# Performance work log

Hardware: AMD Instinct MI355X
Metric: run time of the kernel (lower is better)

Reference implementation:

```python
import jax, jax.numpy as jnp
import numpy as np

B, L, D, H = 2, 2048, 1024, 16
DH = D // H


def setup_inputs() -> dict:
    key = jax.random.key(0)
    ks = jax.random.split(key, 5)
    bound = 1.0 / D ** 0.5
    x = jax.random.normal(ks[0], (B, L, D), dtype=jnp.float32)
    # causal mask: 0 means masked out
    mask = jnp.tril(jnp.ones((L, L), dtype=jnp.int32))[None].repeat(B, axis=0)
    Wq = jax.random.uniform(ks[1], (D, D), jnp.float32, -bound, bound)
    Wk = jax.random.uniform(ks[2], (D, D), jnp.float32, -bound, bound)
    Wv = jax.random.uniform(ks[3], (D, D), jnp.float32, -bound, bound)
    Wo = jax.random.uniform(ks[4], (D, D), jnp.float32, -bound, bound)
    return {"x": x, "mask": mask, "Wq": Wq, "Wk": Wk, "Wv": Wv, "Wo": Wo}


def _split_heads(t):
    # (B, L, D) -> (B, H, L, DH)
    b, l, _ = t.shape
    return t.reshape(b, l, H, DH).transpose(0, 2, 1, 3)


def reference(x, mask, Wq, Wk, Wv, Wo):
    # projections: torch Linear does x @ W.T with W:(out,in)
    q = _split_heads(x @ Wq.T)  # (B,H,L,DH)
    k = _split_heads(x @ Wk.T)
    v = _split_heads(x @ Wv.T)
    scores = jnp.einsum('bhqd,bhkd->bhqk', q, k) / jnp.sqrt(jnp.float32(DH))
    m = mask[:, None, :, :]  # (B,1,L,L)
    scores = jnp.where(m == 0, jnp.float32(-jnp.inf), scores)
    attn = jax.nn.softmax(scores, axis=-1)
    out = jnp.einsum('bhqk,bhkd->bhqd', attn, v)  # (B,H,L,DH)
    out = out.transpose(0, 2, 1, 3).reshape(x.shape[0], x.shape[1], D)
    return out @ Wo.T
```

## Files before the change

kernel.cpp:

```cpp
#include <hip/hip_runtime.h>
#include <stdint.h>


typedef unsigned short u16;
typedef __attribute__((ext_vector_type(8))) short short8;
typedef __attribute__((ext_vector_type(4))) float f32x4;
typedef __attribute__((ext_vector_type(4))) unsigned int uint4v;

#define NEG_BIG (-1e30f)
#define QSCALE 0.18033688011112042f

__device__ __forceinline__ f32x4 mfma16(short8 a, short8 b, f32x4 c) {
    return __builtin_amdgcn_mfma_f32_16x16x32_bf16(a, b, c, 0, 0, 0);
}

__device__ __forceinline__ u16 f2bf(float f) {
    uint32_t u = __float_as_uint(f);
    u += 0x7fffu + ((u >> 16) & 1u);
    return (u16)(u >> 16);
}

#if __has_builtin(__builtin_amdgcn_cvt_pk_bf16_f32)
__device__ __forceinline__ unsigned int f2bf_pk(float a, float b) {
    return __builtin_bit_cast(unsigned int, __builtin_amdgcn_cvt_pk_bf16_f32(a, b));
}
#else
__device__ __forceinline__ unsigned int f2bf_pk(float a, float b) {
    return (unsigned int)f2bf(a) | ((unsigned int)f2bf(b) << 16);
}
#endif

__device__ __forceinline__ void load_lds_16B(const u16* g, u16* lds_base) {
    __builtin_amdgcn_global_load_lds(
        (__attribute__((address_space(1))) void*)(uintptr_t)(const void*)g,
        (__attribute__((address_space(3))) void*)lds_base,
        16, 0, 0);
}

__global__ __launch_bounds__(256) void cvt_kernel(
    const float* __restrict__ x, const float* __restrict__ wq, const float* __restrict__ wk,
    const float* __restrict__ wv, const float* __restrict__ wo, u16* __restrict__ dst)
{
    const int gid = blockIdx.x * 256 + threadIdx.x;
    const float* src; size_t off;
    if (gid < 524288)      { src = x;  off = (size_t)gid * 8; }
    else if (gid < 655360) { src = wq; off = (size_t)(gid - 524288) * 8; }
    else if (gid < 786432) { src = wk; off = (size_t)(gid - 655360) * 8; }
    else if (gid < 917504) { src = wv; off = (size_t)(gid - 786432) * 8; }
    else                   { src = wo; off = (size_t)(gid - 917504) * 8; }
    float4 a = *(const float4*)(src + off);
    float4 b = *(const float4*)(src + off + 4);
    uint4v u = { f2bf_pk(a.x, a.y), f2bf_pk(a.z, a.w),
                 f2bf_pk(b.x, b.y), f2bf_pk(b.z, b.w) };
    *(uint4v*)(dst + (size_t)gid * 8) = u;
}

__device__ __forceinline__ void gemm_bt_128x128_bk64(
    const u16* __restrict__ A, const u16* __restrict__ Bw,
    u16* at, u16* bt, int m0, int n0, f32x4 acc[4][4])
{
    const int tid  = threadIdx.x;
    const int w    = tid >> 6, lane = tid & 63;
    const int quad = lane >> 4, l15 = lane & 15;
    const int wm   = (w >> 1) * 64, wn = (w & 1) * 64;
    const int srow = lane >> 3;
    const int sch  = lane & 7;

    for (int k0 = 0; k0 < 1024; k0 += 64) {
#pragma unroll
        for (int c = 0; c < 4; ++c) {
            int row = w * 32 + c * 8 + srow;
            int g   = sch ^ (row & 7);
            load_lds_16B(A  + (size_t)(m0 + row) * 1024 + k0 + g * 8, at + (w * 32 + c * 8) * 64);
            load_lds_16B(Bw + (size_t)(n0 + row) * 1024 + k0 + g * 8, bt + (w * 32 + c * 8) * 64);
        }
        __syncthreads();
#pragma unroll
        for (int ks = 0; ks < 2; ++ks) {
            short8 af[4], bf[4];
#pragma unroll
            for (int rf = 0; rf < 4; ++rf) {
                int ra = wm + rf * 16 + l15, pa = (ks * 4 + quad) ^ (ra & 7);
                af[rf] = *(const short8*)(at + ra * 64 + pa * 8);
                int rb = wn + rf * 16 + l15, pb = (ks * 4 + quad) ^ (rb & 7);
                bf[rf] = *(const short8*)(bt + rb * 64 + pb * 8);
            }
#pragma unroll
            for (int rf = 0; rf < 4; ++rf)
#pragma unroll
                for (int cf = 0; cf < 4; ++cf)
                    acc[rf][cf] = mfma16(af[rf], bf[cf], acc[rf][cf]);
        }
        __syncthreads();
    }
}

__global__ __launch_bounds__(256, 3) void qkv_gemm(
    const u16* __restrict__ xb, const u16* __restrict__ Wq, const u16* __restrict__ Wk,
    const u16* __restrict__ Wv, u16* __restrict__ qbuf, u16* __restrict__ kbuf,
    u16* __restrict__ vtbuf)
{
    __shared__ __align__(16) u16 at[128 * 64];
    __shared__ __align__(16) u16 bt[128 * 64];
    const int m0  = blockIdx.x * 128;
    const int by  = blockIdx.y;
    const int sel = by >> 3;
    const int n0  = (by & 7) * 128;
    const u16* Wsel = sel == 0 ? Wq : (sel == 1 ? Wk : Wv);

    f32x4 acc[4][4];
    const f32x4 z = {0.f, 0.f, 0.f, 0.f};
#pragma unroll
    for (int i = 0; i < 4; ++i)
#pragma unroll
        for (int j = 0; j < 4; ++j) acc[i][j] = z;

    gemm_bt_128x128_bk64(xb, Wsel, at, bt, m0, n0, acc);

    const int tid  = threadIdx.x, w = tid >> 6, lane = tid & 63;
    const int quad = lane >> 4, l15 = lane & 15;
    const int wm   = (w >> 1) * 64, wn = (w & 1) * 64;

    if (sel < 2) {
        u16* dst = sel == 0 ? qbuf : kbuf;
        const float scl = sel == 0 ? QSCALE : 1.0f;
#pragma unroll
        for (int rf = 0; rf < 4; ++rf)
#pragma unroll
            for (int cf = 0; cf < 4; ++cf) {
                int n = n0 + wn + cf * 16 + l15;
                int h = n >> 6, dh = n & 63;
#pragma unroll
                for (int r = 0; r < 4; ++r) {
                    int m = m0 + wm + rf * 16 + quad * 4 + r;
                    int b = m >> 11, l = m & 2047;
                    dst[(((size_t)(b * 16 + h)) * 2048 + l) * 64 + dh] = f2bf(acc[rf][cf][r] * scl);
                }
            }
    } else {
#pragma unroll
        for (int rf = 0; rf < 4; ++rf)
#pragma unroll
            for (int cf = 0; cf < 4; ++cf) {
                int n = n0 + wn + cf * 16 + l15;
                int h = n >> 6, dh = n & 63;
                int m = m0 + wm + rf * 16 + quad * 4;
                int b = m >> 11, l = m & 2047;
                ushort4 pk;
                pk.x = f2bf(acc[rf][cf][0]);
                pk.y = f2bf(acc[rf][cf][1]);
                pk.z = f2bf(acc[rf][cf][2]);
                pk.w = f2bf(acc[rf][cf][3]);
                *(ushort4*)(vtbuf + (((size_t)(b * 16 + h)) * 64 + dh) * 2048 + l) = pk;
            }
    }
}

__global__ __launch_bounds__(256, 4) void attn_kernel(
    const u16* __restrict__ qbuf, const u16* __restrict__ kbuf,
    const u16* __restrict__ vtbuf, u16* __restrict__ attn)
{
    __shared__ __align__(16) u16 kt[2][64 * 64];
    __shared__ __align__(16) u16 vt[2][64 * 64];
    __shared__ __align__(16) u16 pt[4 * 16 * 64];

    const int tid  = threadIdx.x, w = tid >> 6, lane = tid & 63;
    const int quad = lane >> 4, l15 = lane & 15;
    const int bh   = blockIdx.y;
    const int jq   = ((blockIdx.y >> 3) & 1) ? (int)blockIdx.x : (31 - (int)blockIdx.x);
    const int q0   = jq * 64;
    const int qw   = q0 + w * 16;

    const u16* qbase = qbuf  + (size_t)bh * 2048 * 64;
    const u16* kbase = kbuf  + (size_t)bh * 2048 * 64;
    const u16* vbase = vtbuf + (size_t)bh * 64 * 2048;
    u16* pw = pt + w * (16 * 64);
    const int b = bh >> 4, h = bh & 15;

    const f32x4 z = {0.f, 0.f, 0.f, 0.f};

    short8 qf[2];
#pragma unroll
    for (int ks = 0; ks < 2; ++ks)
        qf[ks] = *(const short8*)(qbase + (size_t)(qw + l15) * 64 + ks * 32 + quad * 8);

    f32x4 o[4];
    float mrun = NEG_BIG, lrun = 0.f;
#pragma unroll
    for (int df = 0; df < 4; ++df) o[df] = z;

    auto stage = [&](int t, int buf) {
        const int k0 = t * 64;
#pragma unroll
        for (int c = 0; c < 2; ++c) {
            int row = w * 16 + c * 8 + (lane >> 3);
            int g   = (lane & 7) ^ (row & 7);
            load_lds_16B(kbase + (size_t)(k0 + row) * 64 + g * 8, kt[buf] + (w * 16 + c * 8) * 64);
            load_lds_16B(vbase + (size_t)row * 2048 + k0 + g * 8, vt[buf] + (w * 16 + c * 8) * 64);
        }
    };

    const int ntiles = jq + 1;
    stage(0, 0);
    for (int t = 0; t < ntiles; ++t) {
        __syncthreads();
        if (t + 1 < ntiles) stage(t + 1, (t + 1) & 1);
        const int k0 = t * 64;
        if (k0 <= qw + 15) {
            const u16* ktb = kt[t & 1];
            const u16* vtb = vt[t & 1];
            f32x4 st[4];
#pragma unroll
            for (int nf = 0; nf < 4; ++nf) st[nf] = z;
#pragma unroll
            for (int ks = 0; ks < 2; ++ks)
#pragma unroll
                for (int nf = 0; nf < 4; ++nf) {
                    int row = nf * 16 + l15;
                    int ph  = (ks * 4 + quad) ^ (row & 7);
                    short8 kf = *(const short8*)(ktb + row * 64 + ph * 8);
                    st[nf] = mfma16(kf, qf[ks], st[nf]);
                }
            if (k0 + 63 > qw) {
                int qrow = qw + l15;
#pragma unroll
                for (int nf = 0; nf < 4; ++nf)
#pragma unroll
                    for (int r = 0; r < 4; ++r) {
                        int key = k0 + nf * 16 + quad * 4 + r;
                        if (key > qrow) st[nf][r] = NEG_BIG;
                    }
            }
            {
                float mx = st[0][0];
#pragma unroll
                for (int nf = 0; nf < 4; ++nf)
#pragma unroll
                    for (int r = 0; r < 4; ++r) mx = fmaxf(mx, st[nf][r]);
                mx = fmaxf(mx, __shfl_xor(mx, 16));
                mx = fmaxf(mx, __shfl_xor(mx, 32));
                float mnew = fmaxf(mrun, mx);
                float alpha = exp2f(mrun - mnew);
                float sum = 0.f;
#pragma unroll
                for (int nf = 0; nf < 4; ++nf)
#pragma unroll
                    for (int r = 0; r < 4; ++r) {
                        float p = exp2f(st[nf][r] - mnew);
                        st[nf][r] = p;
                        sum += p;
                    }
                sum += __shfl_xor(sum, 16);
                sum += __shfl_xor(sum, 32);
                lrun = lrun * alpha + sum;
                mrun = mnew;
#pragma unroll
                for (int df = 0; df < 4; ++df) o[df] *= alpha;
            }
#pragma unroll
            for (int nf = 0; nf < 4; ++nf) {
                int ph = (nf * 2 + (quad >> 1)) ^ (l15 & 7);
                uint2 pk2;
                pk2.x = f2bf_pk(st[nf][0], st[nf][1]);
                pk2.y = f2bf_pk(st[nf][2], st[nf][3]);
                *(uint2*)(pw + l15 * 64 + ph * 8 + (quad & 1) * 4) = pk2;
            }
#pragma unroll
            for (int ks2 = 0; ks2 < 2; ++ks2) {
                int phb = (ks2 * 4 + quad) ^ (l15 & 7);
                short8 pb = *(const short8*)(pw + l15 * 64 + phb * 8);
#pragma unroll
                for (int df = 0; df < 4; ++df) {
                    int row = df * 16 + l15;
                    int ph  = (ks2 * 4 + quad) ^ (row & 7);
                    short8 vf = *(const short8*)(vtb + row * 64 + ph * 8);
                    o[df] = mfma16(vf, pb, o[df]);
                }
            }
        }
    }

    {
        float inv = 1.f / lrun;
        int qrow = qw + l15;
        u16* obase = attn + ((size_t)(b * 2048 + qrow)) * 1024 + h * 64;
#pragma unroll
        for (int df = 0; df < 4; ++df)
#pragma unroll
            for (int r = 0; r < 4; ++r) {
                int dh = df * 16 + quad * 4 + r;
                obase[dh] = f2bf(o[df][r] * inv);
            }
    }
}

__global__ __launch_bounds__(256, 3) void oproj_gemm(
    const u16* __restrict__ attn, const u16* __restrict__ Wo, float* __restrict__ out)
{
    __shared__ __align__(16) u16 at[128 * 64];
    __shared__ __align__(16) u16 bt[64 * 64];
    const int m0 = blockIdx.x * 128;
    const int n0 = blockIdx.y * 64;

    const int tid  = threadIdx.x, w = tid >> 6, lane = tid & 63;
    const int quad = lane >> 4, l15 = lane & 15;
    const int wm   = (w >> 1) * 64, wn = (w & 1) * 32;
    const int srow = lane >> 3, sch = lane & 7;

    f32x4 acc[4][2];
    const f32x4 z = {0.f, 0.f, 0.f, 0.f};
#pragma unroll
    for (int i = 0; i < 4; ++i)
#pragma unroll
        for (int j = 0; j < 2; ++j) acc[i][j] = z;

    for (int k0 = 0; k0 < 1024; k0 += 64) {
#pragma unroll
        for (int c = 0; c < 4; ++c) {
            int row = w * 32 + c * 8 + srow;
            int g   = sch ^ (row & 7);
            load_lds_16B(attn + (size_t)(m0 + row) * 1024 + k0 + g * 8, at + (w * 32 + c * 8) * 64);
        }
#pragma unroll
        for (int c = 0; c < 2; ++c) {
            int row = w * 16 + c * 8 + srow;
            int g   = sch ^ (row & 7);
            load_lds_16B(Wo + (size_t)(n0 + row) * 1024 + k0 + g * 8, bt + (w * 16 + c * 8) * 64);
        }
        __syncthreads();
#pragma unroll
        for (int ks = 0; ks < 2; ++ks) {
            short8 af[4], bf[2];
#pragma unroll
            for (int rf = 0; rf < 4; ++rf) {
                int ra = wm + rf * 16 + l15, pa = (ks * 4 + quad) ^ (ra & 7);
                af[rf] = *(const short8*)(at + ra * 64 + pa * 8);
            }
#pragma unroll
            for (int cf = 0; cf < 2; ++cf) {
                int rb = wn + cf * 16 + l15, pb = (ks * 4 + quad) ^ (rb & 7);
                bf[cf] = *(const short8*)(bt + rb * 64 + pb * 8);
            }
#pragma unroll
            for (int rf = 0; rf < 4; ++rf)
#pragma unroll
                for (int cf = 0; cf < 2; ++cf)
                    acc[rf][cf] = mfma16(af[rf], bf[cf], acc[rf][cf]);
        }
        __syncthreads();
    }

#pragma unroll
    for (int rf = 0; rf < 4; ++rf)
#pragma unroll
        for (int cf = 0; cf < 2; ++cf) {
            int n = n0 + wn + cf * 16 + l15;
#pragma unroll
            for (int r = 0; r < 4; ++r) {
                int m = m0 + wm + rf * 16 + quad * 4 + r;
                out[(size_t)m * 1024 + n] = acc[rf][cf][r];
            }
        }
}

extern "C" void kernel_launch(void* const* d_in, const int* in_sizes, int n_in,
                              void* d_out, int out_size, void* d_ws, size_t ws_size,
                              hipStream_t stream) {
    const float* x  = (const float*)d_in[0];
    const float* Wq = (const float*)d_in[2];
    const float* Wk = (const float*)d_in[3];
    const float* Wv = (const float*)d_in[4];
    const float* Wo = (const float*)d_in[5];

    u16* ws    = (u16*)d_ws;
    const size_t M = 1024 * 1024;
    u16* qbuf  = ws;
    u16* kbuf  = ws + 4 * M;
    u16* vtb   = ws + 8 * M;
    u16* attnb = ws + 12 * M;
    u16* cvtb  = ws + 16 * M;
    u16* xb    = cvtb;
    u16* wqb   = cvtb + 4 * M;
    u16* wkb   = cvtb + 5 * M;
    u16* wvb   = cvtb + 6 * M;
    u16* wob   = cvtb + 7 * M;
    float* out = (float*)d_out;

    cvt_kernel<<<4096, 256, 0, stream>>>(x, Wq, Wk, Wv, Wo, cvtb);
    qkv_gemm<<<dim3(32, 24), 256, 0, stream>>>(xb, wqb, wkb, wvb, qbuf, kbuf, vtb);
    attn_kernel<<<dim3(32, 32), 256, 0, stream>>>(qbuf, kbuf, vtb, attnb);
    oproj_gemm<<<dim3(32, 16), 256, 0, stream>>>(attnb, wob, out);
}
```

Measured before the change: 210.0 us.

## Balance causal attention work by pairing query blocks and splitting long chains

Each attention block now does roughly equal work. A short query tile is paired with the first half of a long query tile's key range, and a second block processes the other half. That second half is written as partial output plus running max and sum, and a new merge kernel combines the two halves into the final attention output. The goal is to remove the triangular load imbalance of causal attention. The cost is an extra kernel launch, partial-result traffic, and storing partial outputs in bf16 before the merge, which costs some precision.

```diff
diff --git a/kernel.cpp b/kernel.cpp
--- a/kernel.cpp
+++ b/kernel.cpp
@@ -18,6 +18,10 @@
     uint32_t u = __float_as_uint(f);
     u += 0x7fffu + ((u >> 16) & 1u);
     return (u16)(u >> 16);
+}
+
+__device__ __forceinline__ float bf2f(u16 v) {
+    return __uint_as_float((uint32_t)v << 16);
 }
 
 #if __has_builtin(__builtin_amdgcn_cvt_pk_bf16_f32)
@@ -156,9 +160,91 @@
     }
 }
 
+
+struct Chain {
+    short8 qf[2];
+    f32x4  o[4];
+    float  m, l;
+};
+
+__device__ __forceinline__ void attn_visit(
+    const u16* ktb, const u16* vtb, u16* pw,
+    Chain& c, int k0, int qrow, bool diag, int quad, int l15)
+{
+    const f32x4 z = {0.f, 0.f, 0.f, 0.f};
+    f32x4 st[4];
+#pragma unroll
+    for (int nf = 0; nf < 4; ++nf) st[nf] = z;
+#pragma unroll
+    for (int ks = 0; ks < 2; ++ks)
+#pragma unroll
+        for (int nf = 0; nf < 4; ++nf) {
+            int row = nf * 16 + l15;
+            int ph  = (ks * 4 + quad) ^ (row & 7);
+            short8 kf = *(const short8*)(ktb + row * 64 + ph * 8);
+            st[nf] = mfma16(kf, c.qf[ks], st[nf]);
+        }
+    if (diag) {
+#pragma unroll
+        for (int nf = 0; nf < 4; ++nf)
+#pragma unroll
+            for (int r = 0; r < 4; ++r) {
+                int key = k0 + nf * 16 + quad * 4 + r;
+                if (key > qrow) st[nf][r] = NEG_BIG;
+            }
+    }
+    {
+        float mx = st[0][0];
+#pragma unroll
+        for (int nf = 0; nf < 4; ++nf)
+#pragma unroll
+            for (int r = 0; r < 4; ++r) mx = fmaxf(mx, st[nf][r]);
+        mx = fmaxf(mx, __shfl_xor(mx, 16));
+        mx = fmaxf(mx, __shfl_xor(mx, 32));
+        float mnew = fmaxf(c.m, mx);
+        float alpha = exp2f(c.m - mnew);
+        float sum = 0.f;
+#pragma unroll
+        for (int nf = 0; nf < 4; ++nf)
+#pragma unroll
+            for (int r = 0; r < 4; ++r) {
+                float p = exp2f(st[nf][r] - mnew);
+                st[nf][r] = p;
+                sum += p;
+            }
+        sum += __shfl_xor(sum, 16);
+        sum += __shfl_xor(sum, 32);
+        c.l = c.l * alpha + sum;
+        c.m = mnew;
+#pragma unroll
+        for (int df = 0; df < 4; ++df) c.o[df] *= alpha;
+    }
+#pragma unroll
+    for (int nf = 0; nf < 4; ++nf) {
+        int ph = (nf * 2 + (quad >> 1)) ^ (l15 & 7);
+        uint2 pk2;
+        pk2.x = f2bf_pk(st[nf][0], st[nf][1]);
+        pk2.y = f2bf_pk(st[nf][2], st[nf][3]);
+        *(uint2*)(pw + l15 * 64 + ph * 8 + (quad & 1) * 4) = pk2;
+    }
+#pragma unroll
+    for (int ks2 = 0; ks2 < 2; ++ks2) {
+        int phb = (ks2 * 4 + quad) ^ (l15 & 7);
+        short8 pb = *(const short8*)(pw + l15 * 64 + phb * 8);
+#pragma unroll
+        for (int df = 0; df < 4; ++df) {
+            int row = df * 16 + l15;
+            int ph  = (ks2 * 4 + quad) ^ (row & 7);
+            short8 vf = *(const short8*)(vtb + row * 64 + ph * 8);
+            c.o[df] = mfma16(vf, pb, c.o[df]);
+        }
+    }
+}
+
 __global__ __launch_bounds__(256, 4) void attn_kernel(
     const u16* __restrict__ qbuf, const u16* __restrict__ kbuf,
-    const u16* __restrict__ vtbuf, u16* __restrict__ attn)
+    const u16* __restrict__ vtbuf, u16* __restrict__ attn,
+    u16* __restrict__ po, float* __restrict__ pm, float* __restrict__ pl)
 {
     __shared__ __align__(16) u16 kt[2][64 * 64];
     __shared__ __align__(16) u16 vt[2][64 * 64];
@@ -167,27 +253,18 @@
     const int tid  = threadIdx.x, w = tid >> 6, lane = tid & 63;
     const int quad = lane >> 4, l15 = lane & 15;
     const int bh   = blockIdx.y;
-    const int jq   = ((blockIdx.y >> 3) & 1) ? (int)blockIdx.x : (31 - (int)blockIdx.x);
-    const int q0   = jq * 64;
-    const int qw   = q0 + w * 16;
+    const int a    = blockIdx.x >> 1;
+    const int role = blockIdx.x & 1;
+    const int jqS  = a, jqB = 31 - a;
 
     const u16* qbase = qbuf  + (size_t)bh * 2048 * 64;
     const u16* kbase = kbuf  + (size_t)bh * 2048 * 64;
     const u16* vbase = vtbuf + (size_t)bh * 64 * 2048;
     u16* pw = pt + w * (16 * 64);
     const int b = bh >> 4, h = bh & 15;
+    const int rowi = w * 16 + l15;
 
     const f32x4 z = {0.f, 0.f, 0.f, 0.f};
-
-    short8 qf[2];
-#pragma unroll
-    for (int ks = 0; ks < 2; ++ks)
-        qf[ks] = *(const short8*)(qbase + (size_t)(qw + l15) * 64 + ks * 32 + quad * 8);
-
-    f32x4 o[4];
-    float mrun = NEG_BIG, lrun = 0.f;
-#pragma unroll
-    for (int df = 0; df < 4; ++df) o[df] = z;
 
     auto stage = [&](int t, int buf) {
         const int k0 = t * 64;
@@ -200,98 +277,109 @@
         }
     };
 
-    const int ntiles = jq + 1;
-    stage(0, 0);
-    for (int t = 0; t < ntiles; ++t) {
-        __syncthreads();
-        if (t + 1 < ntiles) stage(t + 1, (t + 1) & 1);
-        const int k0 = t * 64;
-        if (k0 <= qw + 15) {
+    auto load_q = [&](int jq, Chain& c) {
+        int qw = jq * 64 + w * 16;
+#pragma unroll
+        for (int ks = 0; ks < 2; ++ks)
+            c.qf[ks] = *(const short8*)(qbase + (size_t)(qw + l15) * 64 + ks * 32 + quad * 8);
+        c.m = NEG_BIG; c.l = 0.f;
+#pragma unroll
+        for (int df = 0; df < 4; ++df) c.o[df] = z;
+    };
+
+    if (role == 0) {
+        Chain cS, cB;
+        load_q(jqS, cS);
+        load_q(jqB, cB);
+        const int tS = a, tB = 15 - a;
+        const int T0 = tS > tB ? tS : tB;
+        stage(0, 0);
+        for (int t = 0; t <= T0; ++t) {
+            __syncthreads();
+            if (t < T0) stage(t + 1, (t + 1) & 1);
             const u16* ktb = kt[t & 1];
             const u16* vtb = vt[t & 1];
-            f32x4 st[4];
-#pragma unroll
-            for (int nf = 0; nf < 4; ++nf) st[nf] = z;
-#pragma unroll
-            for (int ks = 0; ks < 2; ++ks)
-#pragma unroll
-                for (int nf = 0; nf < 4; ++nf) {
-                    int row = nf * 16 + l15;
-                    int ph  = (ks * 4 + quad) ^ (row & 7);
-                    short8 kf = *(const short8*)(ktb + row * 64 + ph * 8);
-                    st[nf] = mfma16(kf, qf[ks], st[nf]);
-                }
-            if (k0 + 63 > qw) {
-                int qrow = qw + l15;
-#pragma unroll
-                for (int nf = 0; nf < 4; ++nf)
-#pragma unroll
-                    for (int r = 0; r < 4; ++r) {
-                        int key = k0 + nf * 16 + quad * 4 + r;
-                        if (key > qrow) st[nf][r] = NEG_BIG;
-                    }
-            }
-            {
-                float mx = st[0][0];
-#pragma unroll
-                for (int nf = 0; nf < 4; ++nf)
-#pragma unroll
-                    for (int r = 0; r < 4; ++r) mx = fmaxf(mx, st[nf][r]);
-                mx = fmaxf(mx, __shfl_xor(mx, 16));
-                mx = fmaxf(mx, __shfl_xor(mx, 32));
-                float mnew = fmaxf(mrun, mx);
-                float alpha = exp2f(mrun - mnew);
-                float sum = 0.f;
-#pragma unroll
-                for (int nf = 0; nf < 4; ++nf)
-#pragma unroll
-                    for (int r = 0; r < 4; ++r) {
-                        float p = exp2f(st[nf][r] - mnew);
-                        st[nf][r] = p;
-                        sum += p;
-                    }
-                sum += __shfl_xor(sum, 16);
-                sum += __shfl_xor(sum, 32);
-                lrun = lrun * alpha + sum;
-                mrun = mnew;
-#pragma unroll
-                for (int df = 0; df < 4; ++df) o[df] *= alpha;
-            }
-#pragma unroll
-            for (int nf = 0; nf < 4; ++nf) {
-                int ph = (nf * 2 + (quad >> 1)) ^ (l15 & 7);
-                uint2 pk2;
-                pk2.x = f2bf_pk(st[nf][0], st[nf][1]);
-                pk2.y = f2bf_pk(st[nf][2], st[nf][3]);
-                *(uint2*)(pw + l15 * 64 + ph * 8 + (quad & 1) * 4) = pk2;
-            }
-#pragma unroll
-            for (int ks2 = 0; ks2 < 2; ++ks2) {
-                int phb = (ks2 * 4 + quad) ^ (l15 & 7);
-                short8 pb = *(const short8*)(pw + l15 * 64 + phb * 8);
-#pragma unroll
-                for (int df = 0; df < 4; ++df) {
-                    int row = df * 16 + l15;
-                    int ph  = (ks2 * 4 + quad) ^ (row & 7);
-                    short8 vf = *(const short8*)(vtb + row * 64 + ph * 8);
-                    o[df] = mfma16(vf, pb, o[df]);
-                }
-            }
-        }
-    }
-
-    {
-        float inv = 1.f / lrun;
-        int qrow = qw + l15;
-        u16* obase = attn + ((size_t)(b * 2048 + qrow)) * 1024 + h * 64;
+            const int k0 = t * 64;
+            if (t <= tB) attn_visit(ktb, vtb, pw, cB, k0, 0, false, quad, l15);
+            if (t <= tS) attn_visit(ktb, vtb, pw, cS, k0, jqS * 64 + rowi, t == tS, quad, l15);
+        }
+        {
+            float inv = 1.f / cS.l;
+            int qrow = jqS * 64 + rowi;
+            u16* obase = attn + ((size_t)(b * 2048 + qrow)) * 1024 + h * 64;
+#pragma unroll
+            for (int df = 0; df < 4; ++df)
+#pragma unroll
+                for (int r = 0; r < 4; ++r)
+                    obase[df * 16 + quad * 4 + r] = f2bf(cS.o[df][r] * inv);
+        }
+        {
+            int p = (bh * 16 + a) * 2 + 0;
+            u16* ob = po + (size_t)p * 4096 + rowi * 64;
+#pragma unroll
+            for (int df = 0; df < 4; ++df)
+#pragma unroll
+                for (int r = 0; r < 4; ++r)
+                    ob[df * 16 + quad * 4 + r] = f2bf(cB.o[df][r]);
+            if (quad == 0) { pm[p * 64 + rowi] = cB.m; pl[p * 64 + rowi] = cB.l; }
+        }
+    } else {
+        Chain cB;
+        load_q(jqB, cB);
+        const int tb = 16 - a, te = 31 - a;
+        stage(tb, tb & 1);
+        for (int t = tb; t <= te; ++t) {
+            __syncthreads();
+            if (t < te) stage(t + 1, (t + 1) & 1);
+            attn_visit(kt[t & 1], vt[t & 1], pw, cB, t * 64, jqB * 64 + rowi, t == te, quad, l15);
+        }
+        int p = (bh * 16 + a) * 2 + 1;
+        u16* ob = po + (size_t)p * 4096 + rowi * 64;
 #pragma unroll
         for (int df = 0; df < 4; ++df)
 #pragma unroll
-            for (int r = 0; r < 4; ++r) {
-                int dh = df * 16 + quad * 4 + r;
-                obase[dh] = f2bf(o[df][r] * inv);
-            }
-    }
+            for (int r = 0; r < 4; ++r)
+                ob[df * 16 + quad * 4 + r] = f2bf(cB.o[df][r]);
+        if (quad == 0) { pm[p * 64 + rowi] = cB.m; pl[p * 64 + rowi] = cB.l; }
+    }
+}
+
+__global__ __launch_bounds__(256) void merge_kernel(
+    const u16* __restrict__ po, const float* __restrict__ pm, const float* __restrict__ pl,
+    u16* __restrict__ attn)
+{
+    const int u   = blockIdx.x;
+    const int bh  = u >> 4, a = u & 15;
+    const int b   = bh >> 4, h = bh & 15;
+    const int jqB = 31 - a;
+    const int row = threadIdx.x >> 2, seg = threadIdx.x & 3;
+    const int p0  = u * 2, p1 = u * 2 + 1;
+
+    float m0 = pm[p0 * 64 + row], m1 = pm[p1 * 64 + row];
+    float l0 = pl[p0 * 64 + row], l1 = pl[p1 * 64 + row];
+    float m  = fmaxf(m0, m1);
+    float w0 = exp2f(m0 - m), w1 = exp2f(m1 - m);
+    float inv = 1.f / (l0 * w0 + l1 * w1);
+    w0 *= inv; w1 *= inv;
+
+    const u16* o0p = po + (size_t)p0 * 4096 + row * 64 + seg * 16;
+    const u16* o1p = po + (size_t)p1 * 4096 + row * 64 + seg * 16;
+    short8 o0a = *(const short8*)(o0p);
+    short8 o0b = *(const short8*)(o0p + 8);
+    short8 o1a = *(const short8*)(o1p);
+    short8 o1b = *(const short8*)(o1p + 8);
+
+    float r[16];
+#pragma unroll
+    for (int j = 0; j < 8; ++j) {
+        r[j]     = bf2f((u16)o0a[j]) * w0 + bf2f((u16)o1a[j]) * w1;
+        r[8 + j] = bf2f((u16)o0b[j]) * w0 + bf2f((u16)o1b[j]) * w1;
+    }
+    uint4v pka = { f2bf_pk(r[0], r[1]), f2bf_pk(r[2], r[3]), f2bf_pk(r[4], r[5]), f2bf_pk(r[6], r[7]) };
+    uint4v pkb = { f2bf_pk(r[8], r[9]), f2bf_pk(r[10], r[11]), f2bf_pk(r[12], r[13]), f2bf_pk(r[14], r[15]) };
+    u16* dst = attn + ((size_t)(b * 2048 + jqB * 64 + row)) * 1024 + h * 64 + seg * 16;
+    *(uint4v*)(dst)     = pka;
+    *(uint4v*)(dst + 8) = pkb;
 }
 
 __global__ __launch_bounds__(256, 3) void oproj_gemm(
@@ -386,8 +474,13 @@
     u16* wob   = cvtb + 7 * M;
     float* out = (float*)d_out;
 
+    u16*   po = cvtb;
+    float* pmv = (float*)(cvtb + 4 * M);
+    float* plv = pmv + 32 * 16 * 2 * 64;
+
     cvt_kernel<<<4096, 256, 0, stream>>>(x, Wq, Wk, Wv, Wo, cvtb);
     qkv_gemm<<<dim3(32, 24), 256, 0, stream>>>(xb, wqb, wkb, wvb, qbuf, kbuf, vtb);
-    attn_kernel<<<dim3(32, 32), 256, 0, stream>>>(qbuf, kbuf, vtb, attnb);
+    attn_kernel<<<dim3(32, 32), 256, 0, stream>>>(qbuf, kbuf, vtb, attnb, po, pmv, plv);
+    merge_kernel<<<512, 256, 0, stream>>>(po, pmv, plv, attnb);
     oproj_gemm<<<dim3(32, 16), 256, 0, stream>>>(attnb, wob, out);
 }
```

Measured after the change: 205.9 us. -2.0%, faster.
